# Optimization experiments

Hardware: AMD Instinct MI355X
Metric: run time of the kernel (lower is better)

Reference implementation:

```python
import jax, jax.numpy as jnp
import numpy as np

NUM_NODES = 50000


def setup_inputs() -> dict:
    key = jax.random.key(0)
    ks = jax.random.split(key, 5)
    d = 128
    E = 600000
    x = jax.random.normal(ks[0], (NUM_NODES, d), dtype=jnp.float32)
    edge_attr = jax.random.normal(ks[1], (E, d), dtype=jnp.float32)
    receivers_idx = jax.random.randint(ks[2], (E,), 0, NUM_NODES)
    # MLP params: Linear(2d -> d), ReLU, Linear(d -> d). Stored as [in, out].
    W1 = jax.random.normal(ks[3], (2 * d, d), dtype=jnp.float32) / np.sqrt(2 * d)
    b1 = jnp.zeros((d,), dtype=jnp.float32)
    W2 = jax.random.normal(ks[4], (d, d), dtype=jnp.float32) / np.sqrt(d)
    b2 = jnp.zeros((d,), dtype=jnp.float32)
    return {"x": x, "edge_attr": edge_attr, "receivers_idx": receivers_idx,
            "W1": W1, "b1": b1, "W2": W2, "b2": b2}


def reference(x, edge_attr, receivers_idx, W1, b1, W2, b2):
    # scatter_add(edge_attr, receivers_idx, dim=0, dim_size=num_nodes)
    agg = jax.ops.segment_sum(edge_attr, receivers_idx, num_segments=NUM_NODES)  # [N, d]
    collected = jnp.concatenate([x, agg], axis=-1)  # [N, 2d]
    h = jax.nn.relu(collected @ W1 + b1)  # [N, d]
    out = h @ W2 + b2                     # [N, d]
    # Original returns Data(x=out, edge_attr=edge_attr, edge_index=edge_index);
    # edge_attr/edge_index pass through unchanged, so return the new node features.
    return out
```

## Files before the change

### kernel.cpp

```cpp
#include <hip/hip_runtime.h>
#include <hip/hip_bf16.h>

#define N_NODES 50000
#define DIM 128
#define N_EDGES 600000
#define MAX_DEG 64

typedef __attribute__((ext_vector_type(8))) short short8;
typedef __attribute__((ext_vector_type(4))) float f32x4;

__device__ __forceinline__ unsigned short f2bf_u(float f) {
    return __bfloat16_as_ushort(__float2bfloat16(f));
}

#define FILL_BLOCKS ((N_EDGES + 255) / 256)
#define PREP_BLOCKS 192

__global__ __launch_bounds__(256) void fill_prep(
    const int* __restrict__ ridx, int* __restrict__ cnt, int* __restrict__ elist,
    const float* __restrict__ W1, const float* __restrict__ W2,
    __hip_bfloat16* __restrict__ W1t, __hip_bfloat16* __restrict__ W2t) {
    int b = blockIdx.x;
    if (b < FILL_BLOCKS) {
        int e = b * 256 + threadIdx.x;
        if (e < N_EDGES) {
            int node = ridx[e];
            int pos = atomicAdd(&cnt[node], 1);
            if (pos < MAX_DEG) elist[(size_t)node * MAX_DEG + pos] = e;
        }
    } else {
        int t = (b - FILL_BLOCKS) * 256 + threadIdx.x;
        if (t < 256 * 128) {
            int k = t >> 7, n = t & 127;
            W1t[n * 256 + k] = __float2bfloat16(W1[t]);
        } else {
            int q = t - 256 * 128;
            int k = q >> 7, n = q & 127;
            W2t[n * 128 + k] = __float2bfloat16(W2[q]);
        }
    }
}

__global__ __launch_bounds__(256) void fused_kernel(
    const float* __restrict__ x,
    const float* __restrict__ edge_attr,
    const int* __restrict__ elist,
    const int* __restrict__ cnt,
    const __hip_bfloat16* __restrict__ W1t,
    const float* __restrict__ b1,
    const __hip_bfloat16* __restrict__ W2t,
    const float* __restrict__ b2,
    float* __restrict__ out) {
    __shared__ __hip_bfloat16 sBuf[128][136];

    const int wave = threadIdx.x >> 6;
    const int lane = threadIdx.x & 63;
    const int quad = lane >> 4;
    const int l16  = lane & 15;
    const int rowBase = blockIdx.x * 128 + wave * 32;

    for (int i = 0; i < 32; i++) {
        const int node = rowBase + i;
        unsigned packed = 0u;
        if (node < N_NODES) {
            int deg = cnt[node];
            deg = deg < MAX_DEG ? deg : MAX_DEG;
            const int* el = elist + (size_t)node * MAX_DEG;
            float sx = 0.f, sy = 0.f;
            int j = 0;
            for (; j + 8 <= deg; j += 8) {
                int4 ea = *reinterpret_cast<const int4*>(el + j);
                int4 eb = *reinterpret_cast<const int4*>(el + j + 4);
                float2 v0 = *reinterpret_cast<const float2*>(edge_attr + (size_t)ea.x * DIM + lane * 2);
                float2 v1 = *reinterpret_cast<const float2*>(edge_attr + (size_t)ea.y * DIM + lane * 2);
                float2 v2 = *reinterpret_cast<const float2*>(edge_attr + (size_t)ea.z * DIM + lane * 2);
                float2 v3 = *reinterpret_cast<const float2*>(edge_attr + (size_t)ea.w * DIM + lane * 2);
                float2 v4 = *reinterpret_cast<const float2*>(edge_attr + (size_t)eb.x * DIM + lane * 2);
                float2 v5 = *reinterpret_cast<const float2*>(edge_attr + (size_t)eb.y * DIM + lane * 2);
                float2 v6 = *reinterpret_cast<const float2*>(edge_attr + (size_t)eb.z * DIM + lane * 2);
                float2 v7 = *reinterpret_cast<const float2*>(edge_attr + (size_t)eb.w * DIM + lane * 2);
                sx += ((v0.x + v1.x) + (v2.x + v3.x)) + ((v4.x + v5.x) + (v6.x + v7.x));
                sy += ((v0.y + v1.y) + (v2.y + v3.y)) + ((v4.y + v5.y) + (v6.y + v7.y));
            }
            if (j + 4 <= deg) {
                int4 ea = *reinterpret_cast<const int4*>(el + j);
                float2 v0 = *reinterpret_cast<const float2*>(edge_attr + (size_t)ea.x * DIM + lane * 2);
                float2 v1 = *reinterpret_cast<const float2*>(edge_attr + (size_t)ea.y * DIM + lane * 2);
                float2 v2 = *reinterpret_cast<const float2*>(edge_attr + (size_t)ea.z * DIM + lane * 2);
                float2 v3 = *reinterpret_cast<const float2*>(edge_attr + (size_t)ea.w * DIM + lane * 2);
                sx += (v0.x + v1.x) + (v2.x + v3.x);
                sy += (v0.y + v1.y) + (v2.y + v3.y);
                j += 4;
            }
            for (; j < deg; j++) {
                int e0 = el[j];
                float2 v0 = *reinterpret_cast<const float2*>(edge_attr + (size_t)e0 * DIM + lane * 2);
                sx += v0.x;
                sy += v0.y;
            }
            packed = ((unsigned)f2bf_u(sy) << 16) | (unsigned)f2bf_u(sx);
        }
        *reinterpret_cast<unsigned*>(&sBuf[wave * 32 + i][lane * 2]) = packed;
    }

    f32x4 accH[2][8] = {};
#pragma unroll
    for (int ks = 0; ks < 8; ks++) {
        const int k0 = ks * 32 + quad * 8;
        short8 a[2];
        if (ks < 4) {
#pragma unroll
            for (int rt = 0; rt < 2; rt++) {
                int row = rowBase + rt * 16 + l16;
                row = row < N_NODES ? row : N_NODES - 1;
                const float* xp = x + (size_t)row * DIM + k0;
                f32x4 u = *reinterpret_cast<const f32x4*>(xp);
                f32x4 v = *reinterpret_cast<const f32x4*>(xp + 4);
                short8 av = { (short)f2bf_u(u[0]), (short)f2bf_u(u[1]),
                              (short)f2bf_u(u[2]), (short)f2bf_u(u[3]),
                              (short)f2bf_u(v[0]), (short)f2bf_u(v[1]),
                              (short)f2bf_u(v[2]), (short)f2bf_u(v[3]) };
                a[rt] = av;
            }
        } else {
#pragma unroll
            for (int rt = 0; rt < 2; rt++) {
                int r = wave * 32 + rt * 16 + l16;
                a[rt] = *reinterpret_cast<const short8*>(&sBuf[r][k0 - 128]);
            }
        }
#pragma unroll
        for (int nt = 0; nt < 8; nt++) {
            short8 b = *reinterpret_cast<const short8*>(W1t + (nt * 16 + l16) * 256 + k0);
            accH[0][nt] = __builtin_amdgcn_mfma_f32_16x16x32_bf16(a[0], b, accH[0][nt], 0, 0, 0);
            accH[1][nt] = __builtin_amdgcn_mfma_f32_16x16x32_bf16(a[1], b, accH[1][nt], 0, 0, 0);
        }
    }

#pragma unroll
    for (int nt = 0; nt < 8; nt++) {
        const float bias = b1[nt * 16 + l16];
#pragma unroll
        for (int rt = 0; rt < 2; rt++) {
#pragma unroll
            for (int i = 0; i < 4; i++) {
                float v = accH[rt][nt][i] + bias;
                v = v > 0.0f ? v : 0.0f;
                int r = wave * 32 + rt * 16 + quad * 4 + i;
                sBuf[r][nt * 16 + l16] = __float2bfloat16(v);
            }
        }
    }

    f32x4 accO[2][8] = {};
#pragma unroll
    for (int ks = 0; ks < 4; ks++) {
        const int k0 = ks * 32 + quad * 8;
        short8 a[2];
#pragma unroll
        for (int rt = 0; rt < 2; rt++) {
            int r = wave * 32 + rt * 16 + l16;
            a[rt] = *reinterpret_cast<const short8*>(&sBuf[r][k0]);
        }
#pragma unroll
        for (int nt = 0; nt < 8; nt++) {
            short8 b = *reinterpret_cast<const short8*>(W2t + (nt * 16 + l16) * 128 + k0);
            accO[0][nt] = __builtin_amdgcn_mfma_f32_16x16x32_bf16(a[0], b, accO[0][nt], 0, 0, 0);
            accO[1][nt] = __builtin_amdgcn_mfma_f32_16x16x32_bf16(a[1], b, accO[1][nt], 0, 0, 0);
        }
    }

#pragma unroll
    for (int nt = 0; nt < 8; nt++) {
        const float bias = b2[nt * 16 + l16];
#pragma unroll
        for (int rt = 0; rt < 2; rt++) {
#pragma unroll
            for (int i = 0; i < 4; i++) {
                int row = rowBase + rt * 16 + quad * 4 + i;
                if (row < N_NODES) {
                    out[(size_t)row * DIM + nt * 16 + l16] = accO[rt][nt][i] + bias;
                }
            }
        }
    }
}

extern "C" void kernel_launch(void* const* d_in, const int* in_sizes, int n_in,
                              void* d_out, int out_size, void* d_ws, size_t ws_size,
                              hipStream_t stream) {
    const float* x         = (const float*)d_in[0];
    const float* edge_attr = (const float*)d_in[1];
    const int*   ridx      = (const int*)d_in[2];
    const float* W1        = (const float*)d_in[3];
    const float* b1        = (const float*)d_in[4];
    const float* W2        = (const float*)d_in[5];
    const float* b2        = (const float*)d_in[6];
    float* out = (float*)d_out;

    char* w = (char*)d_ws;
    int* elist = (int*)w;                     w += (size_t)N_NODES * MAX_DEG * 4;
    int* cnt   = (int*)w;                     w += (size_t)N_NODES * 4;
    __hip_bfloat16* W1t = (__hip_bfloat16*)w; w += 256 * 128 * 2;
    __hip_bfloat16* W2t = (__hip_bfloat16*)w;

    hipMemsetAsync(cnt, 0, (size_t)N_NODES * 4, stream);
    fill_prep<<<dim3(FILL_BLOCKS + PREP_BLOCKS), dim3(256), 0, stream>>>(
        ridx, cnt, elist, W1, W2, W1t, W2t);
    fused_kernel<<<dim3((N_NODES + 127) / 128), dim3(256), 0, stream>>>(
        x, edge_attr, elist, cnt, W1t, b1, W2t, b2, out);
}
```

Before: 563.0 us.

## Split fused gather+MLP into separate aggregate and MLP kernels

Moves the neighbor aggregation out of the fused kernel into a dedicated kernel that assigns one wave per node, writing bf16 aggregates to a workspace buffer. The MLP kernel then reads x and agg directly, with 64-row tiles and 16 rows per wave. This is meant to raise occupancy and memory-level parallelism for the latency-bound irregular gather, which previously ran serially over 32 nodes per wave. In exchange it adds an extra global round trip for the aggregate and one more kernel launch.

```diff
diff --git a/kernel.cpp b/kernel.cpp
--- a/kernel.cpp
+++ b/kernel.cpp
@@ -41,99 +41,93 @@
     }
 }
 
-__global__ __launch_bounds__(256) void fused_kernel(
-    const float* __restrict__ x,
+__global__ __launch_bounds__(256) void aggregate_kernel(
     const float* __restrict__ edge_attr,
     const int* __restrict__ elist,
     const int* __restrict__ cnt,
+    __hip_bfloat16* __restrict__ agg) {
+    const int node = blockIdx.x * 4 + (threadIdx.x >> 6);
+    const int lane = threadIdx.x & 63;
+    if (node >= N_NODES) return;
+    int deg = cnt[node];
+    deg = deg < MAX_DEG ? deg : MAX_DEG;
+    const int* el = elist + (size_t)node * MAX_DEG;
+    float sx = 0.f, sy = 0.f;
+    int j = 0;
+    for (; j + 8 <= deg; j += 8) {
+        int4 ea = *reinterpret_cast<const int4*>(el + j);
+        int4 eb = *reinterpret_cast<const int4*>(el + j + 4);
+        float2 v0 = *reinterpret_cast<const float2*>(edge_attr + (size_t)ea.x * DIM + lane * 2);
+        float2 v1 = *reinterpret_cast<const float2*>(edge_attr + (size_t)ea.y * DIM + lane * 2);
+        float2 v2 = *reinterpret_cast<const float2*>(edge_attr + (size_t)ea.z * DIM + lane * 2);
+        float2 v3 = *reinterpret_cast<const float2*>(edge_attr + (size_t)ea.w * DIM + lane * 2);
+        float2 v4 = *reinterpret_cast<const float2*>(edge_attr + (size_t)eb.x * DIM + lane * 2);
+        float2 v5 = *reinterpret_cast<const float2*>(edge_attr + (size_t)eb.y * DIM + lane * 2);
+        float2 v6 = *reinterpret_cast<const float2*>(edge_attr + (size_t)eb.z * DIM + lane * 2);
+        float2 v7 = *reinterpret_cast<const float2*>(edge_attr + (size_t)eb.w * DIM + lane * 2);
+        sx += ((v0.x + v1.x) + (v2.x + v3.x)) + ((v4.x + v5.x) + (v6.x + v7.x));
+        sy += ((v0.y + v1.y) + (v2.y + v3.y)) + ((v4.y + v5.y) + (v6.y + v7.y));
+    }
+    if (j + 4 <= deg) {
+        int4 ea = *reinterpret_cast<const int4*>(el + j);
+        float2 v0 = *reinterpret_cast<const float2*>(edge_attr + (size_t)ea.x * DIM + lane * 2);
+        float2 v1 = *reinterpret_cast<const float2*>(edge_attr + (size_t)ea.y * DIM + lane * 2);
+        float2 v2 = *reinterpret_cast<const float2*>(edge_attr + (size_t)ea.z * DIM + lane * 2);
+        float2 v3 = *reinterpret_cast<const float2*>(edge_attr + (size_t)ea.w * DIM + lane * 2);
+        sx += (v0.x + v1.x) + (v2.x + v3.x);
+        sy += (v0.y + v1.y) + (v2.y + v3.y);
+        j += 4;
+    }
+    for (; j < deg; j++) {
+        int e0 = el[j];
+        float2 v0 = *reinterpret_cast<const float2*>(edge_attr + (size_t)e0 * DIM + lane * 2);
+        sx += v0.x;
+        sy += v0.y;
+    }
+    unsigned packed = ((unsigned)f2bf_u(sy) << 16) | (unsigned)f2bf_u(sx);
+    *reinterpret_cast<unsigned*>(agg + (size_t)node * DIM + lane * 2) = packed;
+}
+
+__global__ __launch_bounds__(256) void mlp_kernel(
+    const float* __restrict__ x,
+    const __hip_bfloat16* __restrict__ agg,
     const __hip_bfloat16* __restrict__ W1t,
     const float* __restrict__ b1,
     const __hip_bfloat16* __restrict__ W2t,
     const float* __restrict__ b2,
     float* __restrict__ out) {
-    __shared__ __hip_bfloat16 sBuf[128][136];
+    __shared__ __hip_bfloat16 sH[64][136];
 
     const int wave = threadIdx.x >> 6;
     const int lane = threadIdx.x & 63;
     const int quad = lane >> 4;
     const int l16  = lane & 15;
-    const int rowBase = blockIdx.x * 128 + wave * 32;
+    const int rowBase = blockIdx.x * 64 + wave * 16;
 
-    for (int i = 0; i < 32; i++) {
-        const int node = rowBase + i;
-        unsigned packed = 0u;
-        if (node < N_NODES) {
-            int deg = cnt[node];
-            deg = deg < MAX_DEG ? deg : MAX_DEG;
-            const int* el = elist + (size_t)node * MAX_DEG;
-            float sx = 0.f, sy = 0.f;
-            int j = 0;
-            for (; j + 8 <= deg; j += 8) {
-                int4 ea = *reinterpret_cast<const int4*>(el + j);
-                int4 eb = *reinterpret_cast<const int4*>(el + j + 4);
-                float2 v0 = *reinterpret_cast<const float2*>(edge_attr + (size_t)ea.x * DIM + lane * 2);
-                float2 v1 = *reinterpret_cast<const float2*>(edge_attr + (size_t)ea.y * DIM + lane * 2);
-                float2 v2 = *reinterpret_cast<const float2*>(edge_attr + (size_t)ea.z * DIM + lane * 2);
-                float2 v3 = *reinterpret_cast<const float2*>(edge_attr + (size_t)ea.w * DIM + lane * 2);
-                float2 v4 = *reinterpret_cast<const float2*>(edge_attr + (size_t)eb.x * DIM + lane * 2);
-                float2 v5 = *reinterpret_cast<const float2*>(edge_attr + (size_t)eb.y * DIM + lane * 2);
-                float2 v6 = *reinterpret_cast<const float2*>(edge_attr + (size_t)eb.z * DIM + lane * 2);
-                float2 v7 = *reinterpret_cast<const float2*>(edge_attr + (size_t)eb.w * DIM + lane * 2);
-                sx += ((v0.x + v1.x) + (v2.x + v3.x)) + ((v4.x + v5.x) + (v6.x + v7.x));
-                sy += ((v0.y + v1.y) + (v2.y + v3.y)) + ((v4.y + v5.y) + (v6.y + v7.y));
-            }
-            if (j + 4 <= deg) {
-                int4 ea = *reinterpret_cast<const int4*>(el + j);
-                float2 v0 = *reinterpret_cast<const float2*>(edge_attr + (size_t)ea.x * DIM + lane * 2);
-                float2 v1 = *reinterpret_cast<const float2*>(edge_attr + (size_t)ea.y * DIM + lane * 2);
-                float2 v2 = *reinterpret_cast<const float2*>(edge_attr + (size_t)ea.z * DIM + lane * 2);
-                float2 v3 = *reinterpret_cast<const float2*>(edge_attr + (size_t)ea.w * DIM + lane * 2);
-                sx += (v0.x + v1.x) + (v2.x + v3.x);
-                sy += (v0.y + v1.y) + (v2.y + v3.y);
-                j += 4;
-            }
-            for (; j < deg; j++) {
-                int e0 = el[j];
-                float2 v0 = *reinterpret_cast<const float2*>(edge_attr + (size_t)e0 * DIM + lane * 2);
-                sx += v0.x;
-                sy += v0.y;
-            }
-            packed = ((unsigned)f2bf_u(sy) << 16) | (unsigned)f2bf_u(sx);
-        }
-        *reinterpret_cast<unsigned*>(&sBuf[wave * 32 + i][lane * 2]) = packed;
-    }
+    int rowA = rowBase + l16;
+    rowA = rowA < N_NODES ? rowA : N_NODES - 1;
 
-    f32x4 accH[2][8] = {};
+    f32x4 accH[8] = {};
 #pragma unroll
     for (int ks = 0; ks < 8; ks++) {
         const int k0 = ks * 32 + quad * 8;
-        short8 a[2];
+        short8 a;
         if (ks < 4) {
-#pragma unroll
-            for (int rt = 0; rt < 2; rt++) {
-                int row = rowBase + rt * 16 + l16;
-                row = row < N_NODES ? row : N_NODES - 1;
-                const float* xp = x + (size_t)row * DIM + k0;
-                f32x4 u = *reinterpret_cast<const f32x4*>(xp);
-                f32x4 v = *reinterpret_cast<const f32x4*>(xp + 4);
-                short8 av = { (short)f2bf_u(u[0]), (short)f2bf_u(u[1]),
-                              (short)f2bf_u(u[2]), (short)f2bf_u(u[3]),
-                              (short)f2bf_u(v[0]), (short)f2bf_u(v[1]),
-                              (short)f2bf_u(v[2]), (short)f2bf_u(v[3]) };
-                a[rt] = av;
-            }
+            const float* xp = x + (size_t)rowA * DIM + k0;
+            f32x4 u = *reinterpret_cast<const f32x4*>(xp);
+            f32x4 v = *reinterpret_cast<const f32x4*>(xp + 4);
+            short8 av = { (short)f2bf_u(u[0]), (short)f2bf_u(u[1]),
+                          (short)f2bf_u(u[2]), (short)f2bf_u(u[3]),
+                          (short)f2bf_u(v[0]), (short)f2bf_u(v[1]),
+                          (short)f2bf_u(v[2]), (short)f2bf_u(v[3]) };
+            a = av;
         } else {
-#pragma unroll
-            for (int rt = 0; rt < 2; rt++) {
-                int r = wave * 32 + rt * 16 + l16;
-                a[rt] = *reinterpret_cast<const short8*>(&sBuf[r][k0 - 128]);
-            }
+            a = *reinterpret_cast<const short8*>(agg + (size_t)rowA * DIM + (k0 - 128));
         }
 #pragma unroll
         for (int nt = 0; nt < 8; nt++) {
             short8 b = *reinterpret_cast<const short8*>(W1t + (nt * 16 + l16) * 256 + k0);
-            accH[0][nt] = __builtin_amdgcn_mfma_f32_16x16x32_bf16(a[0], b, accH[0][nt], 0, 0, 0);
-            accH[1][nt] = __builtin_amdgcn_mfma_f32_16x16x32_bf16(a[1], b, accH[1][nt], 0, 0, 0);
+            accH[nt] = __builtin_amdgcn_mfma_f32_16x16x32_bf16(a, b, accH[nt], 0, 0, 0);
         }
     }
 
@@ -141,32 +135,23 @@
     for (int nt = 0; nt < 8; nt++) {
         const float bias = b1[nt * 16 + l16];
 #pragma unroll
-        for (int rt = 0; rt < 2; rt++) {
-#pragma unroll
-            for (int i = 0; i < 4; i++) {
-                float v = accH[rt][nt][i] + bias;
-                v = v > 0.0f ? v : 0.0f;
-                int r = wave * 32 + rt * 16 + quad * 4 + i;
-                sBuf[r][nt * 16 + l16] = __float2bfloat16(v);
-            }
+        for (int i = 0; i < 4; i++) {
+            float v = accH[nt][i] + bias;
+            v = v > 0.0f ? v : 0.0f;
+            int r = wave * 16 + quad * 4 + i;
+            sH[r][nt * 16 + l16] = __float2bfloat16(v);
         }
     }
 
-    f32x4 accO[2][8] = {};
+    f32x4 accO[8] = {};
 #pragma unroll
     for (int ks = 0; ks < 4; ks++) {
         const int k0 = ks * 32 + quad * 8;
-        short8 a[2];
-#pragma unroll
-        for (int rt = 0; rt < 2; rt++) {
-            int r = wave * 32 + rt * 16 + l16;
-            a[rt] = *reinterpret_cast<const short8*>(&sBuf[r][k0]);
-        }
+        short8 a = *reinterpret_cast<const short8*>(&sH[wave * 16 + l16][k0]);
 #pragma unroll
         for (int nt = 0; nt < 8; nt++) {
             short8 b = *reinterpret_cast<const short8*>(W2t + (nt * 16 + l16) * 128 + k0);
-            accO[0][nt] = __builtin_amdgcn_mfma_f32_16x16x32_bf16(a[0], b, accO[0][nt], 0, 0, 0);
-            accO[1][nt] = __builtin_amdgcn_mfma_f32_16x16x32_bf16(a[1], b, accO[1][nt], 0, 0, 0);
+            accO[nt] = __builtin_amdgcn_mfma_f32_16x16x32_bf16(a, b, accO[nt], 0, 0, 0);
         }
     }
 
@@ -174,13 +159,10 @@
     for (int nt = 0; nt < 8; nt++) {
         const float bias = b2[nt * 16 + l16];
 #pragma unroll
-        for (int rt = 0; rt < 2; rt++) {
-#pragma unroll
-            for (int i = 0; i < 4; i++) {
-                int row = rowBase + rt * 16 + quad * 4 + i;
-                if (row < N_NODES) {
-                    out[(size_t)row * DIM + nt * 16 + l16] = accO[rt][nt][i] + bias;
-                }
+        for (int i = 0; i < 4; i++) {
+            int row = rowBase + quad * 4 + i;
+            if (row < N_NODES) {
+                out[(size_t)row * DIM + nt * 16 + l16] = accO[nt][i] + bias;
             }
         }
     }
@@ -201,12 +183,15 @@
     char* w = (char*)d_ws;
     int* elist = (int*)w;                     w += (size_t)N_NODES * MAX_DEG * 4;
     int* cnt   = (int*)w;                     w += (size_t)N_NODES * 4;
+    __hip_bfloat16* agg = (__hip_bfloat16*)w; w += (size_t)N_NODES * DIM * 2;
     __hip_bfloat16* W1t = (__hip_bfloat16*)w; w += 256 * 128 * 2;
     __hip_bfloat16* W2t = (__hip_bfloat16*)w;
 
     hipMemsetAsync(cnt, 0, (size_t)N_NODES * 4, stream);
     fill_prep<<<dim3(FILL_BLOCKS + PREP_BLOCKS), dim3(256), 0, stream>>>(
         ridx, cnt, elist, W1, W2, W1t, W2t);
-    fused_kernel<<<dim3((N_NODES + 127) / 128), dim3(256), 0, stream>>>(
-        x, edge_attr, elist, cnt, W1t, b1, W2t, b2, out);
+    aggregate_kernel<<<dim3((N_NODES + 3) / 4), dim3(256), 0, stream>>>(
+        edge_attr, elist, cnt, agg);
+    mlp_kernel<<<dim3((N_NODES + 63) / 64), dim3(256), 0, stream>>>(
+        x, agg, W1t, b1, W2t, b2, out);
 }
```

After: 531.5 us. 1.06x faster.
